# Optimization experiments

Measured on AMD Instinct MI355X. Metric: run time of the kernel, lower is better.

## Reference

```python
import jax, jax.numpy as jnp
import numpy as np

KK = 9   # kH * kW
P = 2    # num_points (len(dilations))


def setup_inputs() -> dict:
    key = jax.random.key(0)
    ks = jax.random.split(key, 12)
    N, A, C, OC = 8000, 4000, 256, 256
    R, rH, rW = 64, 64, 64
    inp = {}
    inp["in_core_feats"] = jax.random.normal(ks[0], (N, C), jnp.float32)
    inp["aux_feats"] = jax.random.normal(ks[1], (A, C), jnp.float32)
    # offset MLP: near-zero weights, bias plays role of the dilation-grid init offsets
    inp["off_w"] = 0.01 * jax.random.normal(ks[2], (KK * P * 2, C), jnp.float32)
    inp["off_b"] = 2.0 * jax.random.uniform(ks[3], (KK * P * 2,), jnp.float32) - 1.0
    inp["pw_w"] = 0.01 * jax.random.normal(ks[4], (KK * P, C), jnp.float32)
    inp["pw_b"] = jnp.zeros((KK * P,), jnp.float32)
    inp["mw_w"] = 0.01 * jax.random.normal(ks[5], (KK, C), jnp.float32)
    inp["mw_b"] = jnp.zeros((KK,), jnp.float32)
    inp["weight"] = jax.random.normal(ks[6], (OC, KK * C), jnp.float32) / np.sqrt(KK * C)
    inp["bias"] = 0.01 * jax.random.normal(ks[7], (OC,), jnp.float32)
    inp["id_map"] = jax.random.randint(ks[8], (R, rH, rW), 0, N + A)
    inp["roi_ids"] = jax.random.randint(ks[9], (N,), 0, R)
    inp["pos_ids"] = jax.random.randint(ks[10], (N, 2), 0, rW)
    return inp


def reference(in_core_feats, aux_feats, off_w, off_b, pw_w, pw_b, mw_w, mw_b,
              weight, bias, id_map, roi_ids, pos_ids):
    N, C = in_core_feats.shape
    # predicted sampling locations in RoI (x, y) coords: [N, KK, P, 2]
    conv_xy = (in_core_feats @ off_w.T + off_b).reshape(N, KK, P, 2)
    conv_xy = pos_ids.astype(conv_xy.dtype)[:, None, None, :] + conv_xy
    floor_xy = jnp.floor(conv_xy)
    base_ids = floor_xy.astype(jnp.int32)
    grid = jnp.array([[0, 0], [1, 0], [0, 1], [1, 1]], jnp.int32)
    cids = base_ids[:, :, :, None, :] + grid            # [N, KK, P, 4, 2]
    cx, cy = cids[..., 0], cids[..., 1]
    rH, rW = id_map.shape[1], id_map.shape[2]
    pad = (cx < 0) | (cy < 0) | (cx >= rW) | (cy >= rH)
    cx = jnp.clip(cx, 0, rW - 1)
    cy = jnp.clip(cy, 0, rH - 1)
    gids = id_map[roi_ids[:, None, None, None], cy, cx]  # [N, KK, P, 4]
    pad_idx = N + aux_feats.shape[0]
    gids = jnp.where(pad, pad_idx, gids)
    # interpolation weights, literal translation of the torch indexing
    delta = conv_xy - floor_xy                           # [N, KK, P, 2]
    dstk = jnp.stack([delta, 1.0 - delta], axis=3)       # [N, KK, P, 2, 2]
    x_ids = jnp.array([1, 0, 1, 0])
    y_ids = jnp.array([1, 1, 0, 0])
    w = dstk[:, :, :, 0, :][..., x_ids] * dstk[:, :, :, 1, :][..., y_ids]  # [N, KK, P, 4]
    # point weights (softmax over points) and modulation weights (sigmoid)
    pw = jax.nn.softmax((in_core_feats @ pw_w.T + pw_b).reshape(N, KK, P), axis=2)
    w = pw[..., None] * w
    mw = jax.nn.sigmoid(in_core_feats @ mw_w.T + mw_b)   # [N, KK]
    w = mw[:, :, None, None] * w
    # gather + weighted reduce over points and corners, then dense matmul
    all_feats = jnp.concatenate(
        [in_core_feats, aux_feats, jnp.zeros((1, C), in_core_feats.dtype)], axis=0)
    sampled = jnp.einsum('nkpgc,nkpg->nkc', all_feats[gids], w)  # [N, KK, C]
    out = sampled.reshape(N, KK * C) @ weight.T + bias
    return out
```

## Files before the change

### kernel.cpp

```cpp
#include <hip/hip_runtime.h>

typedef __attribute__((ext_vector_type(8))) short short8;
typedef __attribute__((ext_vector_type(4))) float f32x4;

static __device__ __forceinline__ unsigned short f2b(float f) {
  union { float f; unsigned int u; } v; v.f = f;
  unsigned int u = v.u;
  unsigned int r = (u + 0x7FFFu + ((u >> 16) & 1u)) >> 16;
  return (unsigned short)r;
}
static __device__ __forceinline__ float b2f(unsigned short u) {
  union { unsigned int u; float f; } v; v.u = ((unsigned int)u) << 16;
  return v.f;
}

__global__ __launch_bounds__(256) void setup_kernel(
    const float* __restrict__ core, const float* __restrict__ aux,
    const float* __restrict__ wgt,
    const float* __restrict__ off_w, const float* __restrict__ off_b,
    const float* __restrict__ pw_w,  const float* __restrict__ pw_b,
    const float* __restrict__ mw_w,  const float* __restrict__ mw_b,
    unsigned short* __restrict__ tab, unsigned short* __restrict__ wB,
    float* __restrict__ Wtq, float* __restrict__ bb)
{
  if (blockIdx.x < 3577) {
    const long TAB = 12001L * 256;
    const long WN  = 256L * 2304;
    long i = ((long)blockIdx.x * 256 + threadIdx.x) * 4;
    float4 v;
    unsigned short* dst;
    if (i < TAB) {
      long row = i >> 8;
      if (row < 8000)        v = *(const float4*)(core + i);
      else if (row < 12000)  v = *(const float4*)(aux + (i - 8000L * 256));
      else                   v = make_float4(0.f, 0.f, 0.f, 0.f);
      dst = tab + i;
    } else {
      long j = i - TAB;
      if (j >= WN) return;
      v = *(const float4*)(wgt + j);
      dst = wB + j;
    }
    *(ushort4*)dst = make_ushort4(f2b(v.x), f2b(v.y), f2b(v.z), f2b(v.w));
    return;
  }
  for (int e = threadIdx.x; e < 16384; e += 256) {
    int i = e >> 8;
    int d = (e >> 2) & 63;
    int j = e & 3;
    int c = i * 4 + j;
    float v;
    if (d < 36)      v = off_w[d * 256 + c];
    else if (d < 54) v = pw_w[(d - 36) * 256 + c];
    else if (d < 63) v = mw_w[(d - 54) * 256 + c];
    else             v = 0.f;
    Wtq[(i * 64 + d) * 4 + j] = v;
  }
  if (threadIdx.x < 64) {
    int d = threadIdx.x;
    float b;
    if (d < 36)      b = off_b[d];
    else if (d < 54) b = pw_b[d - 36];
    else if (d < 63) b = mw_b[d - 54];
    else             b = 0.f;
    bb[d] = b;
  }
}

__global__ __launch_bounds__(256) void proj_kernel(
    const float* __restrict__ core,
    const float* __restrict__ Wtq, const float* __restrict__ bb,
    const int* __restrict__ id_map, const int* __restrict__ roi_ids,
    const int* __restrict__ pos_ids,
    int* __restrict__ gids, float* __restrict__ wts)
{
  __shared__ float dots[16][64];
  const int tid  = threadIdx.x;
  const int lane = tid & 63;
  const int wv   = tid >> 6;
  const int nbase = blockIdx.x * 16 + wv * 4;

  float acc0 = 0.f, acc1 = 0.f, acc2 = 0.f, acc3 = 0.f;
  const float4* W4 = (const float4*)Wtq;
  #pragma unroll 4
  for (int i = 0; i < 64; ++i) {
    const float4 w = W4[i * 64 + lane];
    const float4 x0 = *(const float4*)(core + (long)(nbase + 0) * 256 + i * 4);
    const float4 x1 = *(const float4*)(core + (long)(nbase + 1) * 256 + i * 4);
    const float4 x2 = *(const float4*)(core + (long)(nbase + 2) * 256 + i * 4);
    const float4 x3 = *(const float4*)(core + (long)(nbase + 3) * 256 + i * 4);
    acc0 += w.x * x0.x + w.y * x0.y + w.z * x0.z + w.w * x0.w;
    acc1 += w.x * x1.x + w.y * x1.y + w.z * x1.z + w.w * x1.w;
    acc2 += w.x * x2.x + w.y * x2.y + w.z * x2.z + w.w * x2.w;
    acc3 += w.x * x3.x + w.y * x3.y + w.z * x3.z + w.w * x3.w;
  }
  const float b = bb[lane];
  dots[wv * 4 + 0][lane] = acc0 + b;
  dots[wv * 4 + 1][lane] = acc1 + b;
  dots[wv * 4 + 2][lane] = acc2 + b;
  dots[wv * 4 + 3][lane] = acc3 + b;
  __syncthreads();

  #pragma unroll
  for (int round = 0; round < 2; ++round) {
    int task = round * 256 + tid;
    if (task < 288) {
      int nl = task / 18;
      int kp = task - nl * 18;
      int k = kp >> 1, p = kp & 1;
      int n = blockIdx.x * 16 + nl;
      float x = dots[nl][k*4 + p*2 + 0] + (float)pos_ids[n*2 + 0];
      float y = dots[nl][k*4 + p*2 + 1] + (float)pos_ids[n*2 + 1];
      float fx = floorf(x), fy = floorf(y);
      float dx = x - fx, dy = y - fy;
      int bx = (int)fx, by = (int)fy;
      float l0 = dots[nl][36 + k*2], l1 = dots[nl][36 + k*2 + 1];
      float mmax = fmaxf(l0, l1);
      float e0 = __expf(l0 - mmax), e1 = __expf(l1 - mmax);
      float pwv = (p ? e1 : e0) / (e0 + e1);
      float mwv = 1.f / (1.f + __expf(-dots[nl][54 + k]));
      float wb  = pwv * mwv;
      const int* imap = id_map + roi_ids[n] * 4096;
      int base = ((n * 9 + k) * 2 + p) * 4;
      #pragma unroll
      for (int g = 0; g < 4; ++g) {
        int gx = g & 1, gy = g >> 1;
        int cx = bx + gx, cy = by + gy;
        bool pad = ((cx | cy) < 0) | (cx >= 64) | (cy >= 64);
        int cxc = min(max(cx, 0), 63), cyc = min(max(cy, 0), 63);
        int gid = pad ? 12000 : imap[cyc * 64 + cxc];
        float f1 = gx ? dx : dy;
        float f2 = gy ? (1.f - dx) : (1.f - dy);
        gids[base + g] = gid;
        wts[base + g]  = wb * f1 * f2;
      }
    }
  }
}

__global__ __launch_bounds__(256) void gather_kernel(
    const unsigned short* __restrict__ tab,
    const int* __restrict__ gids, const float* __restrict__ wts,
    unsigned short* __restrict__ sampled)
{
  const int lane = threadIdx.x & 63;
  const int wv   = threadIdx.x >> 6;
  const int n    = blockIdx.x * 4 + wv;
  const int c    = lane * 4;
  const long jb  = (long)n * 72;

  int gid[8]; float w[8];
  #pragma unroll
  for (int j = 0; j < 8; ++j) { gid[j] = gids[jb + j]; w[j] = wts[jb + j]; }

  #pragma unroll
  for (int k = 0; k < 9; ++k) {
    ushort4 tv[8];
    #pragma unroll
    for (int j = 0; j < 8; ++j)
      tv[j] = *(const ushort4*)(tab + (long)gid[j] * 256 + c);
    int ngid[8]; float nw[8];
    if (k < 8) {
      #pragma unroll
      for (int j = 0; j < 8; ++j) {
        ngid[j] = gids[jb + (k + 1) * 8 + j];
        nw[j]   = wts[jb + (k + 1) * 8 + j];
      }
    }
    float a0 = 0.f, a1 = 0.f, a2 = 0.f, a3 = 0.f;
    #pragma unroll
    for (int j = 0; j < 8; ++j) {
      a0 += w[j] * b2f(tv[j].x); a1 += w[j] * b2f(tv[j].y);
      a2 += w[j] * b2f(tv[j].z); a3 += w[j] * b2f(tv[j].w);
    }
    *(ushort4*)(sampled + ((long)n * 2304 + k * 256 + c)) =
        make_ushort4(f2b(a0), f2b(a1), f2b(a2), f2b(a3));
    if (k < 8) {
      #pragma unroll
      for (int j = 0; j < 8; ++j) { gid[j] = ngid[j]; w[j] = nw[j]; }
    }
  }
}

__global__ __launch_bounds__(256) void gemm_kernel(
    const unsigned short* __restrict__ S,
    const unsigned short* __restrict__ W,
    const float* __restrict__ bias,
    float* __restrict__ out)
{
  __shared__ __align__(16) unsigned short As[64][72];
  __shared__ __align__(16) unsigned short Bs[64][72];

  const int orig = blockIdx.x;
  const int xcd  = orig & 7;
  const int wgid = (xcd < 4 ? xcd * 63 : 4 * 63 + (xcd - 4) * 62) + (orig >> 3);
  const int m0 = (wgid >> 2) * 64;
  const int n0 = (wgid & 3) * 64;

  const int t    = threadIdx.x;
  const int lane = t & 63;
  const int wv   = t >> 6;
  const int wr   = wv >> 1, wc = wv & 1;

  f32x4 acc[2][2] = {};

  const int srow = t >> 3;
  const int schk = t & 7;

  for (int kt = 0; kt < 36; ++kt) {
    const int k0 = kt * 64;
    const uint4 ra0 = *(const uint4*)(S + (long)(m0 + srow)      * 2304 + k0 + schk * 8);
    const uint4 ra1 = *(const uint4*)(S + (long)(m0 + srow + 32) * 2304 + k0 + schk * 8);
    const uint4 rb0 = *(const uint4*)(W + (long)(n0 + srow)      * 2304 + k0 + schk * 8);
    const uint4 rb1 = *(const uint4*)(W + (long)(n0 + srow + 32) * 2304 + k0 + schk * 8);
    __syncthreads();
    *(uint4*)&As[srow][schk * 8]      = ra0;
    *(uint4*)&As[srow + 32][schk * 8] = ra1;
    *(uint4*)&Bs[srow][schk * 8]      = rb0;
    *(uint4*)&Bs[srow + 32][schk * 8] = rb1;
    __syncthreads();
    #pragma unroll
    for (int kc = 0; kc < 2; ++kc) {
      const int kk = kc * 32 + (lane >> 4) * 8;
      short8 af[2], bf[2];
      af[0] = *(const short8*)&As[wr * 32 + (lane & 15)][kk];
      af[1] = *(const short8*)&As[wr * 32 + 16 + (lane & 15)][kk];
      bf[0] = *(const short8*)&Bs[wc * 32 + (lane & 15)][kk];
      bf[1] = *(const short8*)&Bs[wc * 32 + 16 + (lane & 15)][kk];
      #pragma unroll
      for (int i = 0; i < 2; ++i)
        #pragma unroll
        for (int j = 0; j < 2; ++j)
          acc[i][j] = __builtin_amdgcn_mfma_f32_16x16x32_bf16(af[i], bf[j], acc[i][j], 0, 0, 0);
    }
  }

  #pragma unroll
  for (int i = 0; i < 2; ++i) {
    const int row = m0 + wr * 32 + i * 16 + (lane >> 4) * 4;
    #pragma unroll
    for (int j = 0; j < 2; ++j) {
      const int col = n0 + wc * 32 + j * 16 + (lane & 15);
      const float bs = bias[col];
      #pragma unroll
      for (int r = 0; r < 4; ++r)
        out[(long)(row + r) * 256 + col] = acc[i][j][r] + bs;
    }
  }
}

extern "C" void kernel_launch(void* const* d_in, const int* in_sizes, int n_in,
                              void* d_out, int out_size, void* d_ws, size_t ws_size,
                              hipStream_t stream)
{
  const float* core   = (const float*)d_in[0];
  const float* aux    = (const float*)d_in[1];
  const float* off_w  = (const float*)d_in[2];
  const float* off_b  = (const float*)d_in[3];
  const float* pw_w   = (const float*)d_in[4];
  const float* pw_b   = (const float*)d_in[5];
  const float* mw_w   = (const float*)d_in[6];
  const float* mw_b   = (const float*)d_in[7];
  const float* wgt    = (const float*)d_in[8];
  const float* bias   = (const float*)d_in[9];
  const int* id_map   = (const int*)d_in[10];
  const int* roi_ids  = (const int*)d_in[11];
  const int* pos_ids  = (const int*)d_in[12];
  char* ws = (char*)d_ws;

  unsigned short* tab     = (unsigned short*)(ws);
  unsigned short* wB      = (unsigned short*)(ws + 6144512);
  int*            gd      = (int*)           (ws + 7324160);
  float*          wt      = (float*)         (ws + 9628160);
  unsigned short* sampled = (unsigned short*)(ws + 11932160);
  float*          Wtq     = (float*)         (ws + 48796160);
  float*          bb      = (float*)         (ws + 48861696);
  float* out = (float*)d_out;

  hipLaunchKernelGGL(setup_kernel, dim3(3578), dim3(256), 0, stream,
                     core, aux, wgt, off_w, off_b, pw_w, pw_b, mw_w, mw_b,
                     tab, wB, Wtq, bb);
  hipLaunchKernelGGL(proj_kernel, dim3(500), dim3(256), 0, stream,
                     core, Wtq, bb, id_map, roi_ids, pos_ids, gd, wt);
  hipLaunchKernelGGL(gather_kernel, dim3(2000), dim3(256), 0, stream,
                     tab, gd, wt, sampled);
  hipLaunchKernelGGL(gemm_kernel, dim3(500), dim3(256), 0, stream,
                     sampled, wB, bias, out);
}
```

Measured before the change: 180.8 us.

## Fuse bilinear gather into GEMM, building A tiles in shared memory per tap

The separate gather and GEMM kernels are merged into one kernel. Each block of 512 threads takes 32 output rows, computes the weighted bilinear gather for one tap directly into a shared-memory A tile, loads the matching 256x256 slice of the weight into shared memory, and runs MFMA over all 256 output columns. This removes the write and re-read of the roughly 37 MB bf16 sampled intermediate and one kernel launch. In exchange the grid shrinks to 250 blocks with about 150 KB of shared memory each, and the gather latency is no longer overlapped with MFMA work, so occupancy and latency hiding may suffer.

```diff
diff --git a/kernel.cpp b/kernel.cpp
--- a/kernel.cpp
+++ b/kernel.cpp
@@ -138,114 +138,73 @@
   }
 }
 
-__global__ __launch_bounds__(256) void gather_kernel(
+__global__ __launch_bounds__(512, 2) void gg2_kernel(
     const unsigned short* __restrict__ tab,
+    const unsigned short* __restrict__ W,
     const int* __restrict__ gids, const float* __restrict__ wts,
-    unsigned short* __restrict__ sampled)
-{
-  const int lane = threadIdx.x & 63;
-  const int wv   = threadIdx.x >> 6;
-  const int n    = blockIdx.x * 4 + wv;
-  const int c    = lane * 4;
-  const long jb  = (long)n * 72;
-
-  int gid[8]; float w[8];
-  #pragma unroll
-  for (int j = 0; j < 8; ++j) { gid[j] = gids[jb + j]; w[j] = wts[jb + j]; }
-
-  #pragma unroll
-  for (int k = 0; k < 9; ++k) {
-    ushort4 tv[8];
-    #pragma unroll
-    for (int j = 0; j < 8; ++j)
-      tv[j] = *(const ushort4*)(tab + (long)gid[j] * 256 + c);
-    int ngid[8]; float nw[8];
-    if (k < 8) {
-      #pragma unroll
-      for (int j = 0; j < 8; ++j) {
-        ngid[j] = gids[jb + (k + 1) * 8 + j];
-        nw[j]   = wts[jb + (k + 1) * 8 + j];
-      }
-    }
-    float a0 = 0.f, a1 = 0.f, a2 = 0.f, a3 = 0.f;
-    #pragma unroll
-    for (int j = 0; j < 8; ++j) {
-      a0 += w[j] * b2f(tv[j].x); a1 += w[j] * b2f(tv[j].y);
-      a2 += w[j] * b2f(tv[j].z); a3 += w[j] * b2f(tv[j].w);
-    }
-    *(ushort4*)(sampled + ((long)n * 2304 + k * 256 + c)) =
-        make_ushort4(f2b(a0), f2b(a1), f2b(a2), f2b(a3));
-    if (k < 8) {
-      #pragma unroll
-      for (int j = 0; j < 8; ++j) { gid[j] = ngid[j]; w[j] = nw[j]; }
-    }
-  }
-}
-
-__global__ __launch_bounds__(256) void gemm_kernel(
-    const unsigned short* __restrict__ S,
-    const unsigned short* __restrict__ W,
-    const float* __restrict__ bias,
-    float* __restrict__ out)
-{
-  __shared__ __align__(16) unsigned short As[64][72];
-  __shared__ __align__(16) unsigned short Bs[64][72];
-
-  const int orig = blockIdx.x;
-  const int xcd  = orig & 7;
-  const int wgid = (xcd < 4 ? xcd * 63 : 4 * 63 + (xcd - 4) * 62) + (orig >> 3);
-  const int m0 = (wgid >> 2) * 64;
-  const int n0 = (wgid & 3) * 64;
+    const float* __restrict__ bias, float* __restrict__ out)
+{
+  __shared__ __align__(16) unsigned short As[32][264];
+  __shared__ __align__(16) unsigned short Bs[256][264];
 
   const int t    = threadIdx.x;
+  const int m0   = blockIdx.x * 32;
   const int lane = t & 63;
   const int wv   = t >> 6;
-  const int wr   = wv >> 1, wc = wv & 1;
-
-  f32x4 acc[2][2] = {};
-
-  const int srow = t >> 3;
-  const int schk = t & 7;
-
-  for (int kt = 0; kt < 36; ++kt) {
-    const int k0 = kt * 64;
-    const uint4 ra0 = *(const uint4*)(S + (long)(m0 + srow)      * 2304 + k0 + schk * 8);
-    const uint4 ra1 = *(const uint4*)(S + (long)(m0 + srow + 32) * 2304 + k0 + schk * 8);
-    const uint4 rb0 = *(const uint4*)(W + (long)(n0 + srow)      * 2304 + k0 + schk * 8);
-    const uint4 rb1 = *(const uint4*)(W + (long)(n0 + srow + 32) * 2304 + k0 + schk * 8);
-    __syncthreads();
-    *(uint4*)&As[srow][schk * 8]      = ra0;
-    *(uint4*)&As[srow + 32][schk * 8] = ra1;
-    *(uint4*)&Bs[srow][schk * 8]      = rb0;
-    *(uint4*)&Bs[srow + 32][schk * 8] = rb1;
+  const int wr   = wv >> 2;
+  const int wc   = wv & 3;
+  const int brow = t >> 1;
+  const int bh   = t & 1;
+
+  f32x4 acc[4] = {};
+
+  for (int tap = 0; tap < 9; ++tap) {
     __syncthreads();
     #pragma unroll
-    for (int kc = 0; kc < 2; ++kc) {
+    for (int r = 0; r < 4; ++r) {
+      const int row = wv * 4 + r;
+      const long gb = (long)(m0 + row) * 72 + tap * 8;
+      float a0 = 0.f, a1 = 0.f, a2 = 0.f, a3 = 0.f;
+      #pragma unroll
+      for (int j = 0; j < 8; ++j) {
+        const int   g = gids[gb + j];
+        const float w = wts[gb + j];
+        const ushort4 tv = *(const ushort4*)(tab + (long)g * 256 + lane * 4);
+        a0 += w * b2f(tv.x); a1 += w * b2f(tv.y);
+        a2 += w * b2f(tv.z); a3 += w * b2f(tv.w);
+      }
+      *(ushort4*)&As[row][lane * 4] =
+          make_ushort4(f2b(a0), f2b(a1), f2b(a2), f2b(a3));
+    }
+    {
+      const unsigned short* src = W + (long)brow * 2304 + tap * 256 + bh * 128;
+      #pragma unroll
+      for (int u = 0; u < 16; ++u) {
+        const uint4 v = *(const uint4*)(src + u * 8);
+        *(uint4*)&Bs[brow][bh * 128 + u * 8] = v;
+      }
+    }
+    __syncthreads();
+    #pragma unroll
+    for (int kc = 0; kc < 8; ++kc) {
       const int kk = kc * 32 + (lane >> 4) * 8;
-      short8 af[2], bf[2];
-      af[0] = *(const short8*)&As[wr * 32 + (lane & 15)][kk];
-      af[1] = *(const short8*)&As[wr * 32 + 16 + (lane & 15)][kk];
-      bf[0] = *(const short8*)&Bs[wc * 32 + (lane & 15)][kk];
-      bf[1] = *(const short8*)&Bs[wc * 32 + 16 + (lane & 15)][kk];
-      #pragma unroll
-      for (int i = 0; i < 2; ++i)
-        #pragma unroll
-        for (int j = 0; j < 2; ++j)
-          acc[i][j] = __builtin_amdgcn_mfma_f32_16x16x32_bf16(af[i], bf[j], acc[i][j], 0, 0, 0);
-    }
-  }
-
+      const short8 af = *(const short8*)&As[wr * 16 + (lane & 15)][kk];
+      #pragma unroll
+      for (int nf = 0; nf < 4; ++nf) {
+        const short8 bf = *(const short8*)&Bs[wc * 64 + nf * 16 + (lane & 15)][kk];
+        acc[nf] = __builtin_amdgcn_mfma_f32_16x16x32_bf16(af, bf, acc[nf], 0, 0, 0);
+      }
+    }
+  }
+
+  const int orow = m0 + wr * 16 + (lane >> 4) * 4;
   #pragma unroll
-  for (int i = 0; i < 2; ++i) {
-    const int row = m0 + wr * 32 + i * 16 + (lane >> 4) * 4;
+  for (int nf = 0; nf < 4; ++nf) {
+    const int col = wc * 64 + nf * 16 + (lane & 15);
+    const float bs = bias[col];
     #pragma unroll
-    for (int j = 0; j < 2; ++j) {
-      const int col = n0 + wc * 32 + j * 16 + (lane & 15);
-      const float bs = bias[col];
-      #pragma unroll
-      for (int r = 0; r < 4; ++r)
-        out[(long)(row + r) * 256 + col] = acc[i][j][r] + bs;
-    }
+    for (int r = 0; r < 4; ++r)
+      out[(long)(orow + r) * 256 + col] = acc[nf][r] + bs;
   }
 }
 
@@ -268,13 +227,12 @@
   const int* pos_ids  = (const int*)d_in[12];
   char* ws = (char*)d_ws;
 
-  unsigned short* tab     = (unsigned short*)(ws);
-  unsigned short* wB      = (unsigned short*)(ws + 6144512);
-  int*            gd      = (int*)           (ws + 7324160);
-  float*          wt      = (float*)         (ws + 9628160);
-  unsigned short* sampled = (unsigned short*)(ws + 11932160);
-  float*          Wtq     = (float*)         (ws + 48796160);
-  float*          bb      = (float*)         (ws + 48861696);
+  unsigned short* tab = (unsigned short*)(ws);
+  unsigned short* wB  = (unsigned short*)(ws + 6144512);
+  int*            gd  = (int*)           (ws + 7324160);
+  float*          wt  = (float*)         (ws + 9628160);
+  float*          Wtq = (float*)         (ws + 11932160);
+  float*          bb  = (float*)         (ws + 11997696);
   float* out = (float*)d_out;
 
   hipLaunchKernelGGL(setup_kernel, dim3(3578), dim3(256), 0, stream,
@@ -282,8 +240,6 @@
                      tab, wB, Wtq, bb);
   hipLaunchKernelGGL(proj_kernel, dim3(500), dim3(256), 0, stream,
                      core, Wtq, bb, id_map, roi_ids, pos_ids, gd, wt);
-  hipLaunchKernelGGL(gather_kernel, dim3(2000), dim3(256), 0, stream,
-                     tab, gd, wt, sampled);
-  hipLaunchKernelGGL(gemm_kernel, dim3(500), dim3(256), 0, stream,
-                     sampled, wB, bias, out);
-}
+  hipLaunchKernelGGL(gg2_kernel, dim3(250), dim3(512), 0, stream,
+                     tab, wB, gd, wt, bias, out);
+}
```

Result: slower. 205.8 us (+13.9%).
